# Kernel tuning notes

Measured on AMD Instinct MI355X. Metric: run time of the kernel, lower is better.

## Reference

```python
import jax, jax.numpy as jnp
import numpy as np

H = 2048      # hidden_size
NH = 32       # num attention heads
KVH = 8       # num kv heads
HD = 64       # head_dim
G = NH // KVH # kv groups (4)
EPS = 1e-6
THETA = 1000000.0


def _rms_norm(x, g):
    # normalize over last dim (head_dim)
    var = jnp.mean(jnp.square(x), axis=-1, keepdims=True)
    return x * jax.lax.rsqrt(var + EPS) * g


def _rope(seq_len, dtype):
    inv_freq = 1.0 / (THETA ** (jnp.arange(0, HD, 2, dtype=jnp.float32) / HD))
    pos = jnp.arange(seq_len, dtype=jnp.float32)
    freqs = pos[:, None] * inv_freq[None, :]          # [S, HD/2]
    emb = jnp.concatenate([freqs, freqs], axis=-1)    # [S, HD]
    return jnp.cos(emb).astype(dtype), jnp.sin(emb).astype(dtype)


def _rotate_half(x):
    x1, x2 = jnp.split(x, 2, axis=-1)
    return jnp.concatenate([-x2, x1], axis=-1)


def setup_inputs() -> dict:
    key = jax.random.key(0)
    ks = jax.random.split(key, 8)
    B, S = 1, 2048
    s = lambda fan_in: 1.0 / np.sqrt(fan_in)
    return {
        "hidden_states": jax.random.normal(ks[0], (B, S, H), jnp.float32),
        "Wq": jax.random.normal(ks[1], (H, NH * HD + NH), jnp.float32) * s(H),
        "Wk": jax.random.normal(ks[2], (H, KVH * HD), jnp.float32) * s(H),
        "Wv": jax.random.normal(ks[3], (H, KVH * HD), jnp.float32) * s(H),
        "Wo": jax.random.normal(ks[4], (NH * HD, H), jnp.float32) * s(NH * HD),
        "g_q": jnp.ones((HD,), jnp.float32),
        "g_k": jnp.ones((HD,), jnp.float32),
    }


def reference(hidden_states, Wq, Wk, Wv, Wo, g_q, g_k):
    B, S, _ = hidden_states.shape
    dtype = hidden_states.dtype

    qg = hidden_states @ Wq                              # [B,S,NH*HD+NH]
    k = hidden_states @ Wk                               # [B,S,KVH*HD]
    v = hidden_states @ Wv

    # headwise gate split, grouped per kv head (matches torch view/split)
    qg = qg.reshape(B, S, KVH, G * HD + G)
    q, gate = qg[..., : G * HD], qg[..., G * HD :]       # gate: [B,S,KVH,G]
    gate = gate.reshape(B, S, NH, 1)
    q = q.reshape(B, S, NH, HD).transpose(0, 2, 1, 3)    # [B,NH,S,HD]
    k = k.reshape(B, S, KVH, HD).transpose(0, 2, 1, 3)   # [B,KVH,S,HD]
    v = v.reshape(B, S, KVH, HD).transpose(0, 2, 1, 3)

    q = _rms_norm(q, g_q)
    k = _rms_norm(k, g_k)

    cos, sin = _rope(S, dtype)                           # [S,HD]
    cos, sin = cos[None, None], sin[None, None]
    q = q * cos + _rotate_half(q) * sin
    k = k * cos + _rotate_half(k) * sin

    # GQA: repeat kv heads
    k = jnp.repeat(k, G, axis=1)                         # [B,NH,S,HD]
    v = jnp.repeat(v, G, axis=1)

    # causal SDPA
    scale = 1.0 / np.sqrt(HD)
    scores = jnp.einsum("bhqd,bhkd->bhqk", q, k) * scale
    causal = jnp.tril(jnp.ones((S, S), bool))
    scores = jnp.where(causal[None, None], scores, jnp.finfo(dtype).min)
    probs = jax.nn.softmax(scores, axis=-1)
    attn = jnp.einsum("bhqk,bhkd->bhqd", probs, v)       # [B,NH,S,HD]

    attn = attn.transpose(0, 2, 1, 3)                    # [B,S,NH,HD]
    attn = attn * jax.nn.sigmoid(gate)
    attn = attn.reshape(B, S, NH * HD)
    return attn @ Wo
```

## Files before the change

### kernel.cpp

```cpp
#include <hip/hip_runtime.h>
#include <hip/hip_bf16.h>

#define SLEN 2048
#define HDIM 2048
#define NHEAD 32
#define KVHEAD 8
#define HEADD 64
#define NTOT 3104
#define NPAD 3200

typedef short bh8 __attribute__((ext_vector_type(8)));
typedef float f32x4 __attribute__((ext_vector_type(4)));

#define QSCALE 0.1803368801111204f

__device__ __forceinline__ unsigned short f2bf(float f) {
    union { float f; unsigned int u; } v; v.f = f;
    unsigned int u = v.u;
    return (unsigned short)((u + 0x7fffu + ((u >> 16) & 1u)) >> 16);
}

__device__ __forceinline__ unsigned int cvtpk_bf16(float lo, float hi) {
    unsigned int r;
    asm("v_cvt_pk_bf16_f32 %0, %1, %2" : "=v"(r) : "v"(lo), "v"(hi));
    return r;
}

__device__ __forceinline__ void gl_lds16(const unsigned short* g, unsigned short* l) {
    __builtin_amdgcn_global_load_lds(
        (const __attribute__((address_space(1))) unsigned int*)g,
        (__attribute__((address_space(3))) unsigned int*)l, 16, 0, 0);
}

__global__ void cast_x_k(const float* __restrict__ src, unsigned short* __restrict__ dst, int n) {
    int i = blockIdx.x * blockDim.x + threadIdx.x;
    int base = i * 4;
    if (base < n) {
        float4 f = *(const float4*)(src + base);
        ushort4 o;
        o.x = f2bf(f.x); o.y = f2bf(f.y); o.z = f2bf(f.z); o.w = f2bf(f.w);
        *(ushort4*)(dst + base) = o;
    }
}

__global__ void pack_wt_k(const float* __restrict__ Wq, const float* __restrict__ Wk,
                          const float* __restrict__ Wv, unsigned short* __restrict__ Wt) {
    __shared__ float tile[32][33];
    int n0 = blockIdx.x * 32, k0 = blockIdx.y * 32;
    int t = threadIdx.x;
    for (int i = 0; i < 4; i++) {
        int idx = i * 256 + t;
        int kr = idx >> 5, nc = idx & 31;
        int n = n0 + nc, k = k0 + kr;
        float val = 0.f;
        if (n < 2048)       { int h = n >> 6, d = n & 63; val = Wq[(size_t)k * 2080 + (h >> 2) * 260 + (h & 3) * 64 + d]; }
        else if (n < 2080)  { int h = n - 2048;           val = Wq[(size_t)k * 2080 + (h >> 2) * 260 + 256 + (h & 3)]; }
        else if (n < 2592)  { val = Wk[(size_t)k * 512 + (n - 2080)]; }
        else if (n < 3104)  { val = Wv[(size_t)k * 512 + (n - 2592)]; }
        tile[kr][nc] = val;
    }
    __syncthreads();
    for (int i = 0; i < 4; i++) {
        int idx = i * 256 + t;
        int nr = idx >> 5, kc = idx & 31;
        Wt[(size_t)(n0 + nr) * HDIM + (k0 + kc)] = f2bf(tile[kc][nr]);
    }
}

__global__ void pack_wot_k(const float* __restrict__ Wo, unsigned short* __restrict__ Wt) {
    __shared__ float tile[32][33];
    int n0 = blockIdx.x * 32, k0 = blockIdx.y * 32;
    int t = threadIdx.x;
    for (int i = 0; i < 4; i++) {
        int idx = i * 256 + t;
        int kr = idx >> 5, nc = idx & 31;
        tile[kr][nc] = Wo[(size_t)(k0 + kr) * 2048 + (n0 + nc)];
    }
    __syncthreads();
    for (int i = 0; i < 4; i++) {
        int idx = i * 256 + t;
        int nr = idx >> 5, kc = idx & 31;
        Wt[(size_t)(n0 + nr) * 2048 + (k0 + kc)] = f2bf(tile[kc][nr]);
    }
}

__global__ __launch_bounds__(256) void gemm_nt64_k(const unsigned short* __restrict__ A,
                                                   const unsigned short* __restrict__ Bt,
                                                   float* __restrict__ C,
                                                   int ldc, int mtiles) {
    const int K = 2048;
    __shared__ unsigned short As[3][64 * 32];
    __shared__ unsigned short Bs[3][128 * 32];
    int d = blockIdx.x;
    int nwg = gridDim.x;
    int cpx = nwg >> 3;
    int swz = (d & 7) * cpx + (d >> 3);
    int m0 = (swz % mtiles) * 64, n0 = (swz / mtiles) * 128;
    int t = threadIdx.x;
    int w = t >> 6, l = t & 63;
    int wm = (w >> 1) * 32, wn = (w & 1) * 64;
    int lrow = l & 15, lc = l >> 4;
    int rsw = (lrow >> 1) & 3;
    int scol = ((l & 3) ^ ((l >> 3) & 3)) * 8;

    f32x4 acc[2][4];
    #pragma unroll
    for (int i = 0; i < 2; i++)
        #pragma unroll
        for (int j = 0; j < 4; j++)
            acc[i][j] = {0.f, 0.f, 0.f, 0.f};

    const unsigned short* ga = &A[(size_t)(m0 + w * 16 + (l >> 2)) * K + scol];
    const unsigned short* gb = &Bt[(size_t)(n0 + w * 32 + (l >> 2)) * K + scol];

#define STAGE_NT64(s, b) do { \
        gl_lds16(ga + (size_t)(s) * 32,                  &As[b][w * 512]); \
        gl_lds16(gb + (size_t)(s) * 32,                  &Bs[b][(w * 2 + 0) * 512]); \
        gl_lds16(gb + (size_t)(s) * 32 + 16 * (size_t)K, &Bs[b][(w * 2 + 1) * 512]); \
    } while (0)

#define GBODY(rb) do { \
        bh8 af[2], bb[4]; \
        _Pragma("unroll") \
        for (int i = 0; i < 2; i++) \
            af[i] = *(const bh8*)(&As[rb][(wm + i * 16 + lrow) * 32 + ((lc ^ rsw) * 8)]); \
        _Pragma("unroll") \
        for (int j = 0; j < 4; j++) \
            bb[j] = *(const bh8*)(&Bs[rb][(wn + j * 16 + lrow) * 32 + ((lc ^ rsw) * 8)]); \
        _Pragma("unroll") \
        for (int i = 0; i < 2; i++) \
            _Pragma("unroll") \
            for (int j = 0; j < 4; j++) \
                acc[i][j] = __builtin_amdgcn_mfma_f32_16x16x32_bf16(af[i], bb[j], acc[i][j], 0, 0, 0); \
    } while (0)

#define WB3 asm volatile("s_waitcnt vmcnt(3)\n\ts_barrier" ::: "memory")

    STAGE_NT64(0, 0);
    STAGE_NT64(1, 1);
    for (int sb = 0; sb < 60; sb += 3) {
        WB3;
        STAGE_NT64(sb + 2, 2);
        GBODY(0);
        WB3;
        STAGE_NT64(sb + 3, 0);
        GBODY(1);
        WB3;
        STAGE_NT64(sb + 4, 1);
        GBODY(2);
    }
    WB3;
    STAGE_NT64(62, 2);
    GBODY(0);
    WB3;
    STAGE_NT64(63, 0);
    GBODY(1);
    WB3;
    GBODY(2);
    asm volatile("s_waitcnt vmcnt(0)\n\ts_barrier" ::: "memory");
    GBODY(0);
#undef WB3
#undef STAGE_NT64
#undef GBODY
    int col = l & 15, rbase = (l >> 4) * 4;
    for (int i = 0; i < 2; i++)
        for (int j = 0; j < 4; j++)
            #pragma unroll
            for (int r = 0; r < 4; r++)
                C[(size_t)(m0 + wm + i * 16 + rbase + r) * ldc + (n0 + wn + j * 16 + col)] = acc[i][j][r];
}

__global__ void norm_rope_k(const float* __restrict__ QKVG, unsigned short* __restrict__ Qr,
                            unsigned short* __restrict__ Kr,
                            const float* __restrict__ g_q, const float* __restrict__ g_k) {
    int wid = blockIdx.x * (blockDim.x >> 6) + (threadIdx.x >> 6);
    int lane = threadIdx.x & 63;
    int type, s, hh;
    if (wid < SLEN * NHEAD) { type = 0; s = wid >> 5; hh = wid & 31; }
    else                    { int r = wid - SLEN * NHEAD; type = 1; s = r >> 3; hh = r & 7; }
    int col = (type == 0) ? hh * 64 + lane : 2080 + hh * 64 + lane;
    float x = QKVG[(size_t)s * NPAD + col];
    float sq = x * x;
    #pragma unroll
    for (int off = 32; off; off >>= 1) sq += __shfl_xor(sq, off);
    float inv = rsqrtf(sq * (1.f / 64.f) + 1e-6f);
    float g = (type == 0 ? g_q : g_k)[lane];
    float xn = x * inv * g;
    float xp = __shfl_xor(xn, 32);
    float xr = (lane < 32) ? -xp : xp;
    int i = lane & 31;
    float invf = __expf(-(float)i * (0.03125f * 13.815510557964274f));
    float ang = (float)s * invf;
    float c = cosf(ang), sn = sinf(ang);
    float r = xn * c + xr * sn;
    if (type == 0) Qr[((size_t)hh * SLEN + s) * 64 + lane] = f2bf(r * QSCALE);
    else           Kr[((size_t)hh * SLEN + s) * 64 + lane] = f2bf(r);
}

__global__ void vt_k(const float* __restrict__ QKVG, unsigned short* __restrict__ Vt) {
    __shared__ float tile[64][65];
    int s0 = blockIdx.x * 64, hh = blockIdx.y;
    int t = threadIdx.x;
    #pragma unroll
    for (int i = 0; i < 4; i++) {
        int idx = i * 256 + t;
        int sr = idx >> 4, c4 = (idx & 15) * 4;
        float4 f = *(const float4*)(&QKVG[(size_t)(s0 + sr) * NPAD + 2592 + hh * 64 + c4]);
        tile[sr][c4] = f.x; tile[sr][c4 + 1] = f.y; tile[sr][c4 + 2] = f.z; tile[sr][c4 + 3] = f.w;
    }
    __syncthreads();
    #pragma unroll
    for (int i = 0; i < 4; i++) {
        int idx = i * 256 + t;
        int dr = idx >> 4, c4 = (idx & 15) * 4;
        int hb = c4 >> 5, f = (c4 >> 4) & 1, g = (c4 >> 2) & 3;
        int p = (hb * 4 + g) * 8 + f * 4;
        ushort4 o;
        o.x = f2bf(tile[c4][dr]); o.y = f2bf(tile[c4 + 1][dr]);
        o.z = f2bf(tile[c4 + 2][dr]); o.w = f2bf(tile[c4 + 3][dr]);
        *(ushort4*)(&Vt[((size_t)hh * 64 + dr) * SLEN + s0 + p]) = o;
    }
}

__global__ void gate_sig_k(const float* __restrict__ QKVG, float* __restrict__ gate) {
    int i = blockIdx.x * 256 + threadIdx.x;
    int s = i >> 5, h = i & 31;
    float x = QKVG[(size_t)s * NPAD + 2048 + h];
    gate[i] = 1.f / (1.f + __expf(-x));
}

__global__ __launch_bounds__(256) void attn_k(const unsigned short* __restrict__ Qr,
                                              const unsigned short* __restrict__ Kr,
                                              const unsigned short* __restrict__ Vt,
                                              const float* __restrict__ gate,
                                              unsigned short* __restrict__ attn) {
    __shared__ unsigned short Kls[3][64 * 64];
    __shared__ unsigned short Vls[3][64 * 64];
    int d = blockIdx.x;
    int kvh = d & 7;
    int h = kvh * 4 + ((d >> 3) & 3);
    int qt = 31 - (d >> 5);
    int t = threadIdx.x, w = t >> 6, l = t & 63;
    int ql = l & 15, g = l >> 4;
    const float NEGINF = -__builtin_inff();

    const unsigned short* Kh = Kr + (size_t)kvh * SLEN * 64;
    const unsigned short* Vh = Vt + (size_t)kvh * 64 * SLEN;
    const unsigned short* Qh = Qr + (size_t)h * SLEN * 64;
    int lk = g * 8;
    int r8 = l >> 3, c8 = l & 7;
    int cs = 8 * (c8 ^ r8);
    int R0 = w * 16, R1 = w * 16 + 8;
    int rdswz = (ql & 7) << 4;

    int q0 = qt * 64;
    int qrow = q0 + w * 16 + ql;

    bh8 qa0 = *(const bh8*)(Qh + (size_t)qrow * 64 + lk);
    bh8 qa1 = *(const bh8*)(Qh + (size_t)qrow * 64 + 32 + lk);

    f32x4 o[4];
    #pragma unroll
    for (int i = 0; i < 4; i++) o[i] = {0.f, 0.f, 0.f, 0.f};
    float m2 = NEGINF, lsum = 0.f;

    int ntiles = qt + 1;
    {
        gl_lds16(&Kh[(size_t)(0 + R0 + r8) * 64 + cs], &Kls[0][R0 * 64]);
        gl_lds16(&Kh[(size_t)(0 + R1 + r8) * 64 + cs], &Kls[0][R1 * 64]);
        gl_lds16(&Vh[(size_t)(R0 + r8) * SLEN + 0 + cs], &Vls[0][R0 * 64]);
        gl_lds16(&Vh[(size_t)(R1 + r8) * SLEN + 0 + cs], &Vls[0][R1 * 64]);
    }
    if (ntiles > 1) {
        gl_lds16(&Kh[(size_t)(64 + R0 + r8) * 64 + cs], &Kls[1][R0 * 64]);
        gl_lds16(&Kh[(size_t)(64 + R1 + r8) * 64 + cs], &Kls[1][R1 * 64]);
        gl_lds16(&Vh[(size_t)(R0 + r8) * SLEN + 64 + cs], &Vls[1][R0 * 64]);
        gl_lds16(&Vh[(size_t)(R1 + r8) * SLEN + 64 + cs], &Vls[1][R1 * 64]);
    }
    int rd = 0, wr = 2;

    for (int ti = 0; ti < ntiles; ti++) {
        if (ti + 1 < ntiles) asm volatile("s_waitcnt vmcnt(4)\n\ts_barrier" ::: "memory");
        else                 asm volatile("s_waitcnt vmcnt(0)\n\ts_barrier" ::: "memory");
        if (ti + 2 < ntiles) {
            int kv1 = (ti + 2) * 64;
            gl_lds16(&Kh[(size_t)(kv1 + R0 + r8) * 64 + cs], &Kls[wr][R0 * 64]);
            gl_lds16(&Kh[(size_t)(kv1 + R1 + r8) * 64 + cs], &Kls[wr][R1 * 64]);
            gl_lds16(&Vh[(size_t)(R0 + r8) * SLEN + kv1 + cs], &Vls[wr][R0 * 64]);
            gl_lds16(&Vh[(size_t)(R1 + r8) * SLEN + kv1 + cs], &Vls[wr][R1 * 64]);
        }
        const unsigned short* Kb = &Kls[rd][0];
        const unsigned short* Vb = &Vls[rd][0];
        int kv0 = ti * 64;
        f32x4 sct[4];
        __builtin_amdgcn_s_setprio(1);
        #pragma unroll
        for (int nt = 0; nt < 4; nt++) {
            int rb = (nt * 16 + ql) * 128;
            bh8 kb0 = *(const bh8*)(&Kb[(rb + ((g * 16) ^ rdswz)) >> 1]);
            bh8 kb1 = *(const bh8*)(&Kb[(rb + ((64 + g * 16) ^ rdswz)) >> 1]);
            f32x4 a = {0.f, 0.f, 0.f, 0.f};
            a = __builtin_amdgcn_mfma_f32_16x16x32_bf16(kb0, qa0, a, 0, 0, 0);
            a = __builtin_amdgcn_mfma_f32_16x16x32_bf16(kb1, qa1, a, 0, 0, 0);
            sct[nt] = a;
        }
        __builtin_amdgcn_s_setprio(0);
        if (ti == qt) {
            #pragma unroll
            for (int nt = 0; nt < 4; nt++)
                #pragma unroll
                for (int j = 0; j < 4; j++) {
                    int key = kv0 + nt * 16 + 4 * g + j;
                    if (key > qrow) sct[nt][j] = NEGINF;
                }
        }
        float mt0 = fmaxf(fmaxf(sct[0][0], sct[0][1]), fmaxf(sct[0][2], sct[0][3]));
        float mt1 = fmaxf(fmaxf(sct[1][0], sct[1][1]), fmaxf(sct[1][2], sct[1][3]));
        float mt2 = fmaxf(fmaxf(sct[2][0], sct[2][1]), fmaxf(sct[2][2], sct[2][3]));
        float mt3 = fmaxf(fmaxf(sct[3][0], sct[3][1]), fmaxf(sct[3][2], sct[3][3]));
        float mt = fmaxf(fmaxf(mt0, mt1), fmaxf(mt2, mt3));
        mt = fmaxf(mt, __shfl_xor(mt, 16));
        mt = fmaxf(mt, __shfl_xor(mt, 32));
        if (!__all(mt - m2 <= 8.f)) {
            float mnew = fmaxf(m2, mt);
            float resc = __builtin_amdgcn_exp2f(m2 - mnew);
            m2 = mnew;
            lsum *= resc;
            float rf[4];
            #pragma unroll
            for (int j = 0; j < 4; j++) rf[j] = __shfl(resc, 4 * g + j);
            #pragma unroll
            for (int nt = 0; nt < 4; nt++) {
                f32x4 oo = o[nt];
                #pragma unroll
                for (int j = 0; j < 4; j++) oo[j] *= rf[j];
                o[nt] = oo;
            }
        }
        float ps = 0.f;
        #pragma unroll
        for (int nt = 0; nt < 4; nt++)
            #pragma unroll
            for (int j = 0; j < 4; j++) {
                float p = __builtin_amdgcn_exp2f(sct[nt][j] - m2);
                sct[nt][j] = p;
                ps += p;
            }
        ps += __shfl_xor(ps, 16);
        ps += __shfl_xor(ps, 32);
        lsum += ps;
        union { unsigned int u[4]; bh8 v; } pa0, pa1;
        pa0.u[0] = cvtpk_bf16(sct[0][0], sct[0][1]);
        pa0.u[1] = cvtpk_bf16(sct[0][2], sct[0][3]);
        pa0.u[2] = cvtpk_bf16(sct[1][0], sct[1][1]);
        pa0.u[3] = cvtpk_bf16(sct[1][2], sct[1][3]);
        pa1.u[0] = cvtpk_bf16(sct[2][0], sct[2][1]);
        pa1.u[1] = cvtpk_bf16(sct[2][2], sct[2][3]);
        pa1.u[2] = cvtpk_bf16(sct[3][0], sct[3][1]);
        pa1.u[3] = cvtpk_bf16(sct[3][2], sct[3][3]);
        __builtin_amdgcn_s_setprio(1);
        #pragma unroll
        for (int nt = 0; nt < 4; nt++) {
            int rb = (nt * 16 + ql) * 128;
            bh8 vb0 = *(const bh8*)(&Vb[(rb + ((g * 16) ^ rdswz)) >> 1]);
            bh8 vb1 = *(const bh8*)(&Vb[(rb + ((64 + g * 16) ^ rdswz)) >> 1]);
            o[nt] = __builtin_amdgcn_mfma_f32_16x16x32_bf16(pa0.v, vb0, o[nt], 0, 0, 0);
            o[nt] = __builtin_amdgcn_mfma_f32_16x16x32_bf16(pa1.v, vb1, o[nt], 0, 0, 0);
        }
        __builtin_amdgcn_s_setprio(0);
        rd = (rd == 2) ? 0 : rd + 1;
        wr = (wr == 2) ? 0 : wr + 1;
    }

    float gf[4];
    #pragma unroll
    for (int j = 0; j < 4; j++) {
        float ls = __shfl(lsum, 4 * g + j);
        int row = q0 + w * 16 + 4 * g + j;
        gf[j] = gate[row * 32 + h] / ls;
    }
    #pragma unroll
    for (int j = 0; j < 4; j++) {
        int row = q0 + w * 16 + 4 * g + j;
        #pragma unroll
        for (int nt = 0; nt < 4; nt++)
            attn[(size_t)row * 2048 + h * 64 + nt * 16 + ql] = f2bf(o[nt][j] * gf[j]);
    }
}

extern "C" void kernel_launch(void* const* d_in, const int* in_sizes, int n_in,
                              void* d_out, int out_size, void* d_ws, size_t ws_size,
                              hipStream_t stream) {
    const float* hidden = (const float*)d_in[0];
    const float* Wq = (const float*)d_in[1];
    const float* Wk = (const float*)d_in[2];
    const float* Wv = (const float*)d_in[3];
    const float* Wo = (const float*)d_in[4];
    const float* gq = (const float*)d_in[5];
    const float* gk = (const float*)d_in[6];
    float* out = (float*)d_out;
    char* ws = (char*)d_ws;

    unsigned short* X    = (unsigned short*)(ws + 0);
    unsigned short* Wt   = (unsigned short*)(ws + 8388608);
    float*          QKVG = (float*)(ws + 21495808);
    unsigned short* Qr   = (unsigned short*)(ws + 47710208);
    unsigned short* Kr   = (unsigned short*)(ws + 56098816);
    unsigned short* Vt   = (unsigned short*)(ws + 58195968);
    float*          gate = (float*)(ws + 60293120);
    unsigned short* attn = (unsigned short*)(ws + 60555264);
    unsigned short* Wot  = (unsigned short*)(ws + 68943872);

    cast_x_k<<<dim3(4096), dim3(256), 0, stream>>>(hidden, X, SLEN * HDIM);
    pack_wt_k<<<dim3(100, 64), dim3(256), 0, stream>>>(Wq, Wk, Wv, Wt);
    pack_wot_k<<<dim3(64, 64), dim3(256), 0, stream>>>(Wo, Wot);
    gemm_nt64_k<<<dim3(800), dim3(256), 0, stream>>>(X, Wt, QKVG, NPAD, 32);
    norm_rope_k<<<dim3(20480), dim3(256), 0, stream>>>(QKVG, Qr, Kr, gq, gk);
    vt_k<<<dim3(32, 8), dim3(256), 0, stream>>>(QKVG, Vt);
    gate_sig_k<<<dim3(256), dim3(256), 0, stream>>>(QKVG, gate);
    attn_k<<<dim3(1024), dim3(256), 0, stream>>>(Qr, Kr, Vt, gate, attn);
    gemm_nt64_k<<<dim3(512), dim3(256), 0, stream>>>(attn, Wot, out, 2048, 32);
}
```

Before: 168.5 us.

## Use 128x128 split-K QKV GEMM with two partial buffers summed downstream

Replaces the 64x128-tile QKV projection GEMM with a 128x128-tile kernel that splits K into two halves, so the grid keeps 800 workgroups while each tile does more reuse. The two halves write separate fp32 partial outputs, and the norm/rope, V-transpose and gate kernels now read and add both. The larger tile raises arithmetic intensity per LDS load. In exchange it adds an extra 26MB fp32 partial buffer write and read, and it drops from triple to double buffering.

```diff
diff --git a/kernel.cpp b/kernel.cpp
--- a/kernel.cpp
+++ b/kernel.cpp
@@ -82,6 +82,83 @@
         int nr = idx >> 5, kc = idx & 31;
         Wt[(size_t)(n0 + nr) * 2048 + (k0 + kc)] = f2bf(tile[kc][nr]);
     }
+}
+
+__global__ __launch_bounds__(256) void gemm_nt128_k(const unsigned short* __restrict__ A,
+                                                    const unsigned short* __restrict__ Bt,
+                                                    float* __restrict__ C0,
+                                                    float* __restrict__ C1) {
+    const int K = 2048, ldc = NPAD;
+    __shared__ unsigned short As[2][128 * 32];
+    __shared__ unsigned short Bs[2][128 * 32];
+    int d = blockIdx.x;
+    int swz = (d & 7) * 100 + (d >> 3);
+    int half = swz >= 400;
+    int tile = swz - half * 400;
+    int m0 = (tile & 15) * 128, n0 = (tile >> 4) * 128;
+    float* C = half ? C1 : C0;
+    int t = threadIdx.x;
+    int w = t >> 6, l = t & 63;
+    int wm = (w >> 1) * 64, wn = (w & 1) * 64;
+    int lrow = l & 15, lc = l >> 4;
+    int rsw = (lrow >> 1) & 3;
+    int scol = ((l & 3) ^ ((l >> 3) & 3)) * 8;
+    int srowA = w * 32 + (l >> 2);
+
+    f32x4 acc[4][4];
+    #pragma unroll
+    for (int i = 0; i < 4; i++)
+        #pragma unroll
+        for (int j = 0; j < 4; j++)
+            acc[i][j] = {0.f, 0.f, 0.f, 0.f};
+
+    const unsigned short* ga = &A[(size_t)(m0 + srowA) * K + half * 1024 + scol];
+    const unsigned short* gb = &Bt[(size_t)(n0 + srowA) * K + half * 1024 + scol];
+
+#define STAGE128(s, b) do { \
+        const unsigned short* a0 = ga + (size_t)(s) * 32; \
+        const unsigned short* b0 = gb + (size_t)(s) * 32; \
+        gl_lds16(a0,                  &As[b][(w * 2 + 0) * 512]); \
+        gl_lds16(a0 + 16 * (size_t)K, &As[b][(w * 2 + 1) * 512]); \
+        gl_lds16(b0,                  &Bs[b][(w * 2 + 0) * 512]); \
+        gl_lds16(b0 + 16 * (size_t)K, &Bs[b][(w * 2 + 1) * 512]); \
+    } while (0)
+
+#define GBODY128(rb) do { \
+        bh8 af[4], bb[4]; \
+        _Pragma("unroll") \
+        for (int i = 0; i < 4; i++) \
+            af[i] = *(const bh8*)(&As[rb][(wm + i * 16 + lrow) * 32 + ((lc ^ rsw) * 8)]); \
+        _Pragma("unroll") \
+        for (int j = 0; j < 4; j++) \
+            bb[j] = *(const bh8*)(&Bs[rb][(wn + j * 16 + lrow) * 32 + ((lc ^ rsw) * 8)]); \
+        _Pragma("unroll") \
+        for (int i = 0; i < 4; i++) \
+            _Pragma("unroll") \
+            for (int j = 0; j < 4; j++) \
+                acc[i][j] = __builtin_amdgcn_mfma_f32_16x16x32_bf16(af[i], bb[j], acc[i][j], 0, 0, 0); \
+    } while (0)
+
+#define WB0 asm volatile("s_waitcnt vmcnt(0)\n\ts_barrier" ::: "memory")
+
+    STAGE128(0, 0);
+    for (int sb = 0; sb < 32; sb += 2) {
+        WB0;
+        STAGE128(sb + 1, 1);
+        GBODY128(0);
+        WB0;
+        if (sb + 2 < 32) STAGE128(sb + 2, 0);
+        GBODY128(1);
+    }
+#undef WB0
+#undef STAGE128
+#undef GBODY128
+    int col = l & 15, rbase = (l >> 4) * 4;
+    for (int i = 0; i < 4; i++)
+        for (int j = 0; j < 4; j++)
+            #pragma unroll
+            for (int r = 0; r < 4; r++)
+                C[(size_t)(m0 + wm + i * 16 + rbase + r) * ldc + (n0 + wn + j * 16 + col)] = acc[i][j][r];
 }
 
 __global__ __launch_bounds__(256) void gemm_nt64_k(const unsigned short* __restrict__ A,
@@ -170,8 +247,8 @@
                 C[(size_t)(m0 + wm + i * 16 + rbase + r) * ldc + (n0 + wn + j * 16 + col)] = acc[i][j][r];
 }
 
-__global__ void norm_rope_k(const float* __restrict__ QKVG, unsigned short* __restrict__ Qr,
-                            unsigned short* __restrict__ Kr,
+__global__ void norm_rope_k(const float* __restrict__ QKVG, const float* __restrict__ QKVG1,
+                            unsigned short* __restrict__ Qr, unsigned short* __restrict__ Kr,
                             const float* __restrict__ g_q, const float* __restrict__ g_k) {
     int wid = blockIdx.x * (blockDim.x >> 6) + (threadIdx.x >> 6);
     int lane = threadIdx.x & 63;
@@ -179,7 +256,8 @@
     if (wid < SLEN * NHEAD) { type = 0; s = wid >> 5; hh = wid & 31; }
     else                    { int r = wid - SLEN * NHEAD; type = 1; s = r >> 3; hh = r & 7; }
     int col = (type == 0) ? hh * 64 + lane : 2080 + hh * 64 + lane;
-    float x = QKVG[(size_t)s * NPAD + col];
+    size_t idx = (size_t)s * NPAD + col;
+    float x = QKVG[idx] + QKVG1[idx];
     float sq = x * x;
     #pragma unroll
     for (int off = 32; off; off >>= 1) sq += __shfl_xor(sq, off);
@@ -197,7 +275,8 @@
     else           Kr[((size_t)hh * SLEN + s) * 64 + lane] = f2bf(r);
 }
 
-__global__ void vt_k(const float* __restrict__ QKVG, unsigned short* __restrict__ Vt) {
+__global__ void vt_k(const float* __restrict__ QKVG, const float* __restrict__ QKVG1,
+                     unsigned short* __restrict__ Vt) {
     __shared__ float tile[64][65];
     int s0 = blockIdx.x * 64, hh = blockIdx.y;
     int t = threadIdx.x;
@@ -205,8 +284,11 @@
     for (int i = 0; i < 4; i++) {
         int idx = i * 256 + t;
         int sr = idx >> 4, c4 = (idx & 15) * 4;
-        float4 f = *(const float4*)(&QKVG[(size_t)(s0 + sr) * NPAD + 2592 + hh * 64 + c4]);
-        tile[sr][c4] = f.x; tile[sr][c4 + 1] = f.y; tile[sr][c4 + 2] = f.z; tile[sr][c4 + 3] = f.w;
+        size_t off = (size_t)(s0 + sr) * NPAD + 2592 + hh * 64 + c4;
+        float4 f = *(const float4*)(&QKVG[off]);
+        float4 f1 = *(const float4*)(&QKVG1[off]);
+        tile[sr][c4] = f.x + f1.x; tile[sr][c4 + 1] = f.y + f1.y;
+        tile[sr][c4 + 2] = f.z + f1.z; tile[sr][c4 + 3] = f.w + f1.w;
     }
     __syncthreads();
     #pragma unroll
@@ -222,10 +304,12 @@
     }
 }
 
-__global__ void gate_sig_k(const float* __restrict__ QKVG, float* __restrict__ gate) {
+__global__ void gate_sig_k(const float* __restrict__ QKVG, const float* __restrict__ QKVG1,
+                           float* __restrict__ gate) {
     int i = blockIdx.x * 256 + threadIdx.x;
     int s = i >> 5, h = i & 31;
-    float x = QKVG[(size_t)s * NPAD + 2048 + h];
+    size_t idx = (size_t)s * NPAD + 2048 + h;
+    float x = QKVG[idx] + QKVG1[idx];
     gate[i] = 1.f / (1.f + __expf(-x));
 }
 
@@ -401,23 +485,24 @@
     float* out = (float*)d_out;
     char* ws = (char*)d_ws;
 
-    unsigned short* X    = (unsigned short*)(ws + 0);
-    unsigned short* Wt   = (unsigned short*)(ws + 8388608);
-    float*          QKVG = (float*)(ws + 21495808);
-    unsigned short* Qr   = (unsigned short*)(ws + 47710208);
-    unsigned short* Kr   = (unsigned short*)(ws + 56098816);
-    unsigned short* Vt   = (unsigned short*)(ws + 58195968);
-    float*          gate = (float*)(ws + 60293120);
-    unsigned short* attn = (unsigned short*)(ws + 60555264);
-    unsigned short* Wot  = (unsigned short*)(ws + 68943872);
+    unsigned short* X     = (unsigned short*)(ws + 0);
+    unsigned short* Wt    = (unsigned short*)(ws + 8388608);
+    float*          QKVG  = (float*)(ws + 21495808);
+    unsigned short* Qr    = (unsigned short*)(ws + 47710208);
+    unsigned short* Kr    = (unsigned short*)(ws + 56098816);
+    unsigned short* Vt    = (unsigned short*)(ws + 58195968);
+    float*          gate  = (float*)(ws + 60293120);
+    unsigned short* attn  = (unsigned short*)(ws + 60555264);
+    unsigned short* Wot   = (unsigned short*)(ws + 68943872);
+    float*          QKVG1 = (float*)(ws + 77332480);
 
     cast_x_k<<<dim3(4096), dim3(256), 0, stream>>>(hidden, X, SLEN * HDIM);
     pack_wt_k<<<dim3(100, 64), dim3(256), 0, stream>>>(Wq, Wk, Wv, Wt);
     pack_wot_k<<<dim3(64, 64), dim3(256), 0, stream>>>(Wo, Wot);
-    gemm_nt64_k<<<dim3(800), dim3(256), 0, stream>>>(X, Wt, QKVG, NPAD, 32);
-    norm_rope_k<<<dim3(20480), dim3(256), 0, stream>>>(QKVG, Qr, Kr, gq, gk);
-    vt_k<<<dim3(32, 8), dim3(256), 0, stream>>>(QKVG, Vt);
-    gate_sig_k<<<dim3(256), dim3(256), 0, stream>>>(QKVG, gate);
+    gemm_nt128_k<<<dim3(800), dim3(256), 0, stream>>>(X, Wt, QKVG, QKVG1);
+    norm_rope_k<<<dim3(20480), dim3(256), 0, stream>>>(QKVG, QKVG1, Qr, Kr, gq, gk);
+    vt_k<<<dim3(32, 8), dim3(256), 0, stream>>>(QKVG, QKVG1, Vt);
+    gate_sig_k<<<dim3(256), dim3(256), 0, stream>>>(QKVG, QKVG1, gate);
     attn_k<<<dim3(1024), dim3(256), 0, stream>>>(Qr, Kr, Vt, gate, attn);
     gemm_nt64_k<<<dim3(512), dim3(256), 0, stream>>>(attn, Wot, out, 2048, 32);
 }
```

New measurement: 173.0 us. 1.03x slower.

## Split-K the output projection GEMM and fuse post-QKV kernels into one launch

Applied to the files above, without the earlier changes.

The output projection GEMM is split along K into two halves, doubling the workgroup count from 512 to 1024 to fill more CUs, with partial results written to two fp32 buffers and summed by a new vectorized add kernel. The norm/rope, V transpose and gate sigmoid kernels are merged into a single launch dispatched by block index, removing two kernel launches. The split-K adds an extra 16MB read plus 8MB write pass and one more launch, and the fused kernel carries shared memory for all blocks.

```diff
diff --git a/kernel.cpp b/kernel.cpp
--- a/kernel.cpp
+++ b/kernel.cpp
@@ -84,10 +84,12 @@
     }
 }
 
+template<int NST>
 __global__ __launch_bounds__(256) void gemm_nt64_k(const unsigned short* __restrict__ A,
                                                    const unsigned short* __restrict__ Bt,
-                                                   float* __restrict__ C,
-                                                   int ldc, int mtiles) {
+                                                   float* __restrict__ C0,
+                                                   float* __restrict__ C1,
+                                                   int ldc, int mtiles, int ntiles) {
     const int K = 2048;
     __shared__ unsigned short As[3][64 * 32];
     __shared__ unsigned short Bs[3][128 * 32];
@@ -95,7 +97,11 @@
     int nwg = gridDim.x;
     int cpx = nwg >> 3;
     int swz = (d & 7) * cpx + (d >> 3);
-    int m0 = (swz % mtiles) * 64, n0 = (swz / mtiles) * 128;
+    int half = (swz >= ntiles) ? 1 : 0;
+    int tile = swz - half * ntiles;
+    int m0 = (tile % mtiles) * 64, n0 = (tile / mtiles) * 128;
+    float* C = half ? C1 : C0;
+    int koff = half * (NST * 32);
     int t = threadIdx.x;
     int w = t >> 6, l = t & 63;
     int wm = (w >> 1) * 32, wn = (w & 1) * 64;
@@ -110,8 +116,8 @@
         for (int j = 0; j < 4; j++)
             acc[i][j] = {0.f, 0.f, 0.f, 0.f};
 
-    const unsigned short* ga = &A[(size_t)(m0 + w * 16 + (l >> 2)) * K + scol];
-    const unsigned short* gb = &Bt[(size_t)(n0 + w * 32 + (l >> 2)) * K + scol];
+    const unsigned short* ga = &A[(size_t)(m0 + w * 16 + (l >> 2)) * K + koff + scol];
+    const unsigned short* gb = &Bt[(size_t)(n0 + w * 32 + (l >> 2)) * K + koff + scol];
 
 #define STAGE_NT64(s, b) do { \
         gl_lds16(ga + (size_t)(s) * 32,                  &As[b][w * 512]); \
@@ -138,27 +144,45 @@
 
     STAGE_NT64(0, 0);
     STAGE_NT64(1, 1);
-    for (int sb = 0; sb < 60; sb += 3) {
+    if constexpr (NST == 64) {
+        for (int sb = 0; sb < 60; sb += 3) {
+            WB3;
+            STAGE_NT64(sb + 2, 2);
+            GBODY(0);
+            WB3;
+            STAGE_NT64(sb + 3, 0);
+            GBODY(1);
+            WB3;
+            STAGE_NT64(sb + 4, 1);
+            GBODY(2);
+        }
         WB3;
-        STAGE_NT64(sb + 2, 2);
+        STAGE_NT64(62, 2);
         GBODY(0);
         WB3;
-        STAGE_NT64(sb + 3, 0);
+        STAGE_NT64(63, 0);
         GBODY(1);
         WB3;
-        STAGE_NT64(sb + 4, 1);
         GBODY(2);
-    }
-    WB3;
-    STAGE_NT64(62, 2);
-    GBODY(0);
-    WB3;
-    STAGE_NT64(63, 0);
-    GBODY(1);
-    WB3;
-    GBODY(2);
-    asm volatile("s_waitcnt vmcnt(0)\n\ts_barrier" ::: "memory");
-    GBODY(0);
+        asm volatile("s_waitcnt vmcnt(0)\n\ts_barrier" ::: "memory");
+        GBODY(0);
+    } else {
+        for (int sb = 0; sb < 30; sb += 3) {
+            WB3;
+            STAGE_NT64(sb + 2, 2);
+            GBODY(0);
+            WB3;
+            STAGE_NT64(sb + 3, 0);
+            GBODY(1);
+            WB3;
+            STAGE_NT64(sb + 4, 1);
+            GBODY(2);
+        }
+        WB3;
+        GBODY(0);
+        asm volatile("s_waitcnt vmcnt(0)\n\ts_barrier" ::: "memory");
+        GBODY(1);
+    }
 #undef WB3
 #undef STAGE_NT64
 #undef GBODY
@@ -170,63 +194,74 @@
                 C[(size_t)(m0 + wm + i * 16 + rbase + r) * ldc + (n0 + wn + j * 16 + col)] = acc[i][j][r];
 }
 
-__global__ void norm_rope_k(const float* __restrict__ QKVG, unsigned short* __restrict__ Qr,
-                            unsigned short* __restrict__ Kr,
-                            const float* __restrict__ g_q, const float* __restrict__ g_k) {
-    int wid = blockIdx.x * (blockDim.x >> 6) + (threadIdx.x >> 6);
-    int lane = threadIdx.x & 63;
-    int type, s, hh;
-    if (wid < SLEN * NHEAD) { type = 0; s = wid >> 5; hh = wid & 31; }
-    else                    { int r = wid - SLEN * NHEAD; type = 1; s = r >> 3; hh = r & 7; }
-    int col = (type == 0) ? hh * 64 + lane : 2080 + hh * 64 + lane;
-    float x = QKVG[(size_t)s * NPAD + col];
-    float sq = x * x;
-    #pragma unroll
-    for (int off = 32; off; off >>= 1) sq += __shfl_xor(sq, off);
-    float inv = rsqrtf(sq * (1.f / 64.f) + 1e-6f);
-    float g = (type == 0 ? g_q : g_k)[lane];
-    float xn = x * inv * g;
-    float xp = __shfl_xor(xn, 32);
-    float xr = (lane < 32) ? -xp : xp;
-    int i = lane & 31;
-    float invf = __expf(-(float)i * (0.03125f * 13.815510557964274f));
-    float ang = (float)s * invf;
-    float c = cosf(ang), sn = sinf(ang);
-    float r = xn * c + xr * sn;
-    if (type == 0) Qr[((size_t)hh * SLEN + s) * 64 + lane] = f2bf(r * QSCALE);
-    else           Kr[((size_t)hh * SLEN + s) * 64 + lane] = f2bf(r);
-}
-
-__global__ void vt_k(const float* __restrict__ QKVG, unsigned short* __restrict__ Vt) {
+__global__ void addf4_k(const float* __restrict__ a, const float* __restrict__ b,
+                        float* __restrict__ o) {
+    int i = (blockIdx.x * 256 + threadIdx.x) * 4;
+    float4 x = *(const float4*)(a + i);
+    float4 y = *(const float4*)(b + i);
+    float4 r; r.x = x.x + y.x; r.y = x.y + y.y; r.z = x.z + y.z; r.w = x.w + y.w;
+    *(float4*)(o + i) = r;
+}
+
+__global__ void post_qkv_k(const float* __restrict__ QKVG,
+                           unsigned short* __restrict__ Qr, unsigned short* __restrict__ Kr,
+                           unsigned short* __restrict__ Vt, float* __restrict__ gate,
+                           const float* __restrict__ g_q, const float* __restrict__ g_k) {
     __shared__ float tile[64][65];
-    int s0 = blockIdx.x * 64, hh = blockIdx.y;
-    int t = threadIdx.x;
-    #pragma unroll
-    for (int i = 0; i < 4; i++) {
-        int idx = i * 256 + t;
-        int sr = idx >> 4, c4 = (idx & 15) * 4;
-        float4 f = *(const float4*)(&QKVG[(size_t)(s0 + sr) * NPAD + 2592 + hh * 64 + c4]);
-        tile[sr][c4] = f.x; tile[sr][c4 + 1] = f.y; tile[sr][c4 + 2] = f.z; tile[sr][c4 + 3] = f.w;
-    }
-    __syncthreads();
-    #pragma unroll
-    for (int i = 0; i < 4; i++) {
-        int idx = i * 256 + t;
-        int dr = idx >> 4, c4 = (idx & 15) * 4;
-        int hb = c4 >> 5, f = (c4 >> 4) & 1, g = (c4 >> 2) & 3;
-        int p = (hb * 4 + g) * 8 + f * 4;
-        ushort4 o;
-        o.x = f2bf(tile[c4][dr]); o.y = f2bf(tile[c4 + 1][dr]);
-        o.z = f2bf(tile[c4 + 2][dr]); o.w = f2bf(tile[c4 + 3][dr]);
-        *(ushort4*)(&Vt[((size_t)hh * 64 + dr) * SLEN + s0 + p]) = o;
-    }
-}
-
-__global__ void gate_sig_k(const float* __restrict__ QKVG, float* __restrict__ gate) {
-    int i = blockIdx.x * 256 + threadIdx.x;
-    int s = i >> 5, h = i & 31;
-    float x = QKVG[(size_t)s * NPAD + 2048 + h];
-    gate[i] = 1.f / (1.f + __expf(-x));
+    int b = blockIdx.x;
+    if (b < 20480) {
+        int wid = b * 4 + (threadIdx.x >> 6);
+        int lane = threadIdx.x & 63;
+        int type, s, hh;
+        if (wid < SLEN * NHEAD) { type = 0; s = wid >> 5; hh = wid & 31; }
+        else                    { int r = wid - SLEN * NHEAD; type = 1; s = r >> 3; hh = r & 7; }
+        int col = (type == 0) ? hh * 64 + lane : 2080 + hh * 64 + lane;
+        float x = QKVG[(size_t)s * NPAD + col];
+        float sq = x * x;
+        #pragma unroll
+        for (int off = 32; off; off >>= 1) sq += __shfl_xor(sq, off);
+        float inv = rsqrtf(sq * (1.f / 64.f) + 1e-6f);
+        float g = (type == 0 ? g_q : g_k)[lane];
+        float xn = x * inv * g;
+        float xp = __shfl_xor(xn, 32);
+        float xr = (lane < 32) ? -xp : xp;
+        int i = lane & 31;
+        float invf = __expf(-(float)i * (0.03125f * 13.815510557964274f));
+        float ang = (float)s * invf;
+        float c = cosf(ang), sn = sinf(ang);
+        float r = xn * c + xr * sn;
+        if (type == 0) Qr[((size_t)hh * SLEN + s) * 64 + lane] = f2bf(r * QSCALE);
+        else           Kr[((size_t)hh * SLEN + s) * 64 + lane] = f2bf(r);
+    } else if (b < 20736) {
+        int b2 = b - 20480;
+        int hh = b2 >> 5, s0 = (b2 & 31) * 64;
+        int t = threadIdx.x;
+        #pragma unroll
+        for (int i = 0; i < 4; i++) {
+            int idx = i * 256 + t;
+            int sr = idx >> 4, c4 = (idx & 15) * 4;
+            float4 f = *(const float4*)(&QKVG[(size_t)(s0 + sr) * NPAD + 2592 + hh * 64 + c4]);
+            tile[sr][c4] = f.x; tile[sr][c4 + 1] = f.y; tile[sr][c4 + 2] = f.z; tile[sr][c4 + 3] = f.w;
+        }
+        __syncthreads();
+        #pragma unroll
+        for (int i = 0; i < 4; i++) {
+            int idx = i * 256 + t;
+            int dr = idx >> 4, c4 = (idx & 15) * 4;
+            int hb = c4 >> 5, f = (c4 >> 4) & 1, g = (c4 >> 2) & 3;
+            int p = (hb * 4 + g) * 8 + f * 4;
+            ushort4 o;
+            o.x = f2bf(tile[c4][dr]); o.y = f2bf(tile[c4 + 1][dr]);
+            o.z = f2bf(tile[c4 + 2][dr]); o.w = f2bf(tile[c4 + 3][dr]);
+            *(ushort4*)(&Vt[((size_t)hh * 64 + dr) * SLEN + s0 + p]) = o;
+        }
+    } else {
+        int b2 = b - 20736;
+        int i = b2 * 256 + threadIdx.x;
+        int s = i >> 5, h = i & 31;
+        float x = QKVG[(size_t)s * NPAD + 2048 + h];
+        gate[i] = 1.f / (1.f + __expf(-x));
+    }
 }
 
 __global__ __launch_bounds__(256) void attn_k(const unsigned short* __restrict__ Qr,
@@ -401,23 +436,24 @@
     float* out = (float*)d_out;
     char* ws = (char*)d_ws;
 
-    unsigned short* X    = (unsigned short*)(ws + 0);
-    unsigned short* Wt   = (unsigned short*)(ws + 8388608);
-    float*          QKVG = (float*)(ws + 21495808);
-    unsigned short* Qr   = (unsigned short*)(ws + 47710208);
-    unsigned short* Kr   = (unsigned short*)(ws + 56098816);
-    unsigned short* Vt   = (unsigned short*)(ws + 58195968);
-    float*          gate = (float*)(ws + 60293120);
-    unsigned short* attn = (unsigned short*)(ws + 60555264);
-    unsigned short* Wot  = (unsigned short*)(ws + 68943872);
+    unsigned short* X     = (unsigned short*)(ws + 0);
+    unsigned short* Wt    = (unsigned short*)(ws + 8388608);
+    float*          QKVG  = (float*)(ws + 21495808);
+    unsigned short* Qr    = (unsigned short*)(ws + 47710208);
+    unsigned short* Kr    = (unsigned short*)(ws + 56098816);
+    unsigned short* Vt    = (unsigned short*)(ws + 58195968);
+    float*          gate  = (float*)(ws + 60293120);
+    unsigned short* attnb = (unsigned short*)(ws + 60555264);
+    unsigned short* Wot   = (unsigned short*)(ws + 68943872);
+    float*          P1    = (float*)(ws + 77332480);
+    float*          P0    = QKVG;
 
     cast_x_k<<<dim3(4096), dim3(256), 0, stream>>>(hidden, X, SLEN * HDIM);
     pack_wt_k<<<dim3(100, 64), dim3(256), 0, stream>>>(Wq, Wk, Wv, Wt);
     pack_wot_k<<<dim3(64, 64), dim3(256), 0, stream>>>(Wo, Wot);
-    gemm_nt64_k<<<dim3(800), dim3(256), 0, stream>>>(X, Wt, QKVG, NPAD, 32);
-    norm_rope_k<<<dim3(20480), dim3(256), 0, stream>>>(QKVG, Qr, Kr, gq, gk);
-    vt_k<<<dim3(32, 8), dim3(256), 0, stream>>>(QKVG, Vt);
-    gate_sig_k<<<dim3(256), dim3(256), 0, stream>>>(QKVG, gate);
-    attn_k<<<dim3(1024), dim3(256), 0, stream>>>(Qr, Kr, Vt, gate, attn);
-    gemm_nt64_k<<<dim3(512), dim3(256), 0, stream>>>(attn, Wot, out, 2048, 32);
-}
+    gemm_nt64_k<64><<<dim3(800), dim3(256), 0, stream>>>(X, Wt, QKVG, QKVG, NPAD, 32, 800);
+    post_qkv_k<<<dim3(20992), dim3(256), 0, stream>>>(QKVG, Qr, Kr, Vt, gate, gq, gk);
+    attn_k<<<dim3(1024), dim3(256), 0, stream>>>(Qr, Kr, Vt, gate, attnb);
+    gemm_nt64_k<32><<<dim3(1024), dim3(256), 0, stream>>>(attnb, Wot, P0, P1, 2048, 32, 512);
+    addf4_k<<<dim3(4096), dim3(256), 0, stream>>>(P0, P1, out);
+}
```

Measured after the change: 169.9 us. No clear change (+0.8%).
